# Kernel optimization log

Hardware: AMD Instinct MI355X
Metric: run time of the kernel (lower is better)

The kernel has to match this reference:

```python
import jax, jax.numpy as jnp
from jax import lax
import numpy as np

# dims
V, D, T = 30000, 300, 24          # vocab, glove dim, seq len
H = 256                            # tweet_out_size == z_dim
NT, NU = 6000, 4000                # tweet nodes, user nodes
N = NT + NU
F, Z = 512, 256                    # user_feat_size, z_dim
E = 80000
B = 2000                           # batch_size (source tweets)
H1, H2, HEADS = 64, 100, 8
NEG = 0.2                          # GATConv default negative_slope


def setup_inputs() -> dict:
    k = jax.random.split(jax.random.key(0), 32)
    r = lambda i, shape, s=0.05: (s * jax.random.normal(k[i], shape)).astype(jnp.float32)
    return {
        "user_text": jax.random.randint(k[0], (B, T), 0, V),
        "user_feats": jax.random.normal(k[1], (NU, F), jnp.float32),
        "graph_node_features": jax.random.randint(k[2], (NT, T), 0, V),
        "graph_edge_index": jax.random.randint(k[3], (2, E), 0, N),
        "tweet_emb": r(4, (V, D), 0.1),
        "w_ih0": r(5, (3 * H, D)), "w_hh0": r(6, (3 * H, H)),
        "b_ih0": r(7, (3 * H,)), "b_hh0": r(8, (3 * H,)),
        "w_ih1": r(9, (3 * H, H)), "w_hh1": r(10, (3 * H, H)),
        "b_ih1": r(11, (3 * H,)), "b_hh1": r(12, (3 * H,)),
        "h0": r(13, (2, NT, H), 1.0),
        "w_mu": r(14, (Z, F)), "b_mu": r(15, (Z,)),
        "w_lv": r(16, (Z, F)), "b_lv": r(17, (Z,)),
        "w_dec": r(18, (F, Z)), "b_dec": r(19, (F,)),
        "vae_eps": r(20, (NU, Z), 1.0),
        "w1": r(21, (H, HEADS * H1)), "a_src1": r(22, (HEADS, H1)),
        "a_dst1": r(23, (HEADS, H1)), "b1": r(24, (HEADS * H1,)),
        "w2": r(25, (HEADS * H1, H2)), "a_src2": r(26, (1, H2)),
        "a_dst2": r(27, (1, H2)), "b2": r(28, (H2,)),
    }


def _gru_layer(x_seq, h0, w_ih, w_hh, b_ih, b_hh):
    # x_seq: [T, B, in]; torch nn.GRU gate math
    def step(h, x):
        gi = x @ w_ih.T + b_ih
        gh = h @ w_hh.T + b_hh
        i_r, i_z, i_n = jnp.split(gi, 3, axis=-1)
        h_r, h_z, h_n = jnp.split(gh, 3, axis=-1)
        r = jax.nn.sigmoid(i_r + h_r)
        z = jax.nn.sigmoid(i_z + h_z)
        n = jnp.tanh(i_n + r * h_n)
        hn = (1.0 - z) * n + z * h
        return hn, hn
    h_last, out = lax.scan(step, h0, x_seq)
    return out, h_last


def _gat(x, src, dst, w, a_src, a_dst, bias, heads, out_ch, concat):
    # PyG GATConv (eval mode, self-loops already appended)
    n = x.shape[0]
    xp = (x @ w).reshape(n, heads, out_ch)          # [N, H, C]
    as_n = (xp * a_src).sum(-1)                     # [N, H]
    ad_n = (xp * a_dst).sum(-1)
    e = jax.nn.leaky_relu(as_n[src] + ad_n[dst], NEG)          # [E, H]
    emax = jax.ops.segment_max(e, dst, num_segments=n)         # edge-softmax over dst
    ee = jnp.exp(e - emax[dst])
    denom = jax.ops.segment_sum(ee, dst, num_segments=n)
    alpha = ee / denom[dst]
    out = jax.ops.segment_sum(xp[src] * alpha[:, :, None], dst, num_segments=n)
    out = out.reshape(n, heads * out_ch) if concat else out.mean(axis=1)
    return out + bias


def reference(user_text, user_feats, graph_node_features, graph_edge_index,
              tweet_emb, w_ih0, w_hh0, b_ih0, b_hh0, w_ih1, w_hh1, b_ih1, b_hh1,
              h0, w_mu, b_mu, w_lv, b_lv, w_dec, b_dec, vae_eps,
              w1, a_src1, a_dst1, b1, w2, a_src2, a_dst2, b2):
    # --- VAE user embedding ---
    mu = user_feats @ w_mu.T + b_mu
    logvar = user_feats @ w_lv.T + b_lv
    z = mu + jnp.exp(0.5 * logvar) * vae_eps        # reparameterized latent
    rec = z @ w_dec.T + b_dec
    kl_loss = (-0.5 * (1.0 + logvar - mu**2 - jnp.exp(logvar)).sum(-1)).mean()
    rec_loss = ((rec - user_feats) ** 2).mean()
    # --- tweet encoder: embedding lookup + 2-layer GRU ---
    xe = tweet_emb[graph_node_features].transpose(1, 0, 2)     # [T, NT, D]
    out0, _ = _gru_layer(xe, h0[0], w_ih0, w_hh0, b_ih0, b_hh0)
    _, hn = _gru_layer(out0, h0[1], w_ih1, w_hh1, b_ih1, b_hh1)  # [NT, H]
    # --- assemble node features: source tweets, users, other tweets ---
    x_in = jnp.concatenate([hn[:B], z, hn[B:]], axis=0)        # [N, H]
    loops = jnp.arange(x_in.shape[0])
    src = jnp.concatenate([graph_edge_index[0], loops])
    dst = jnp.concatenate([graph_edge_index[1], loops])
    x1 = _gat(x_in, src, dst, w1, a_src1, a_dst1, b1, HEADS, H1, True)
    x2 = _gat(x1, src, dst, w2, a_src2, a_dst2, b2, 1, H2, False)
    return x2, kl_loss, rec_loss
```

## Files before the change

### kernel.cpp

```cpp
#include <hip/hip_runtime.h>

#define V_ 30000
#define D_ 300
#define DP_ 320
#define T_ 24
#define H_ 256
#define NT_ 6000
#define NU_ 4000
#define N_ 10000
#define F_ 512
#define Z_ 256
#define E_ 80000
#define B_ 2000
#define H1_ 64
#define H2_ 100
#define HEADS_ 8
#define E2_ (E_ + N_)

typedef __bf16 bf16_t;
typedef bf16_t bf16x8 __attribute__((ext_vector_type(8)));
typedef float  f32x4  __attribute__((ext_vector_type(4)));

__device__ __forceinline__ void gll16(const bf16_t* g, bf16_t* l)
{
    __builtin_amdgcn_global_load_lds(
        (const __attribute__((address_space(1))) void*)g,
        (__attribute__((address_space(3))) void*)l, 16, 0, 0);
}

struct GCfg {
    const bf16_t* A; const bf16_t* B; const float* bias;
    float* Cf; bf16_t* Cb; int M, N, K, ldc;
    const int* gtok; int t0;
};

template<bool OUTBF>
__global__ __launch_bounds__(256) void mfma_gemm(GCfg g0, GCfg g1)
{
    const GCfg g = blockIdx.z ? g1 : g0;
    __shared__ __align__(16) bf16_t SMEM[16384];
    const int tid  = (int)threadIdx.x;
    const int wave = tid >> 6, lane = tid & 63;
    const int quad = lane >> 4, l16 = lane & 15;
    const int mq = (wave & 1) * 64, nq = (wave >> 1) * 64;

    int bx = (int)blockIdx.x, by = (int)blockIdx.y;
    {
        int gx = (int)gridDim.x, total = gx * (int)gridDim.y;
        if ((total & 7) == 0) {
            int L = by * gx + bx;
            int F = (L & 7) * (total >> 3) + (L >> 3);
            bx = F % gx;
            by = F / gx;
        }
    }
    const int mbase = by * 128, nbase = bx * 128;
    const int M = g.M, N = g.N, K = g.K, ldc = g.ldc;

    const bf16_t* agp[2];
    const bf16_t* bgp[2];
#pragma unroll
    for (int j = 0; j < 2; j++) {
        int i = wave * 128 + j * 64 + lane;
        int c = i >> 7, row = i & 127;
        int r = mbase + row; if (r >= M) r = M - 1;
        int src = g.gtok ? g.gtok[(r % NT_) * T_ + g.t0 + (r / NT_)] : r;
        agp[j] = g.A + (size_t)src * K + c * 8;
        int rb = nbase + row; if (rb >= N) rb = N - 1;
        bgp[j] = g.B + (size_t)rb * K + c * 8;
    }

    f32x4 acc[4][4];
#pragma unroll
    for (int mi = 0; mi < 4; mi++)
#pragma unroll
        for (int ni = 0; ni < 4; ni++) acc[mi][ni] = (f32x4){0.f, 0.f, 0.f, 0.f};

    auto stage = [&](int b, int k0) {
        bf16_t* ab = SMEM + b * 4096 + wave * 1024;
        bf16_t* bb = SMEM + 8192 + b * 4096 + wave * 1024;
        gll16(agp[0] + k0, ab);
        gll16(agp[1] + k0, ab + 512);
        gll16(bgp[0] + k0, bb);
        gll16(bgp[1] + k0, bb + 512);
    };

    const int niter = K >> 5;
    stage(0, 0);
    for (int ks = 0; ks < niter; ks++) {
        __syncthreads();
        if (ks + 1 < niter) stage((ks + 1) & 1, (ks + 1) * 32);
        const bf16_t* Ab = SMEM + (ks & 1) * 4096;
        const bf16_t* Bb = SMEM + 8192 + (ks & 1) * 4096;
        bf16x8 afr[4], bfr[4];
#pragma unroll
        for (int mi = 0; mi < 4; mi++)
            afr[mi] = *(const bf16x8*)(Ab + (size_t)(quad * 128 + mq + mi * 16 + l16) * 8);
#pragma unroll
        for (int ni = 0; ni < 4; ni++)
            bfr[ni] = *(const bf16x8*)(Bb + (size_t)(quad * 128 + nq + ni * 16 + l16) * 8);
#pragma unroll
        for (int mi = 0; mi < 4; mi++)
#pragma unroll
            for (int ni = 0; ni < 4; ni++)
                acc[mi][ni] = __builtin_amdgcn_mfma_f32_16x16x32_bf16(
                    afr[mi], bfr[ni], acc[mi][ni], 0, 0, 0);
    }

    if (OUTBF) {
        __syncthreads();
#pragma unroll
        for (int ni = 0; ni < 4; ni++) {
            int colc = nq + ni * 16 + l16;
            float bv = g.bias ? g.bias[nbase + colc] : 0.f;
            int cc = colc >> 3, off = colc & 7;
#pragma unroll
            for (int mi = 0; mi < 4; mi++)
#pragma unroll
                for (int r = 0; r < 4; r++) {
                    int row = mq + mi * 16 + quad * 4 + r;
                    int sw = (row ^ (row >> 3)) & 7;
                    SMEM[row * 128 + ((cc ^ sw) << 3) + off] =
                        (bf16_t)(acc[mi][ni][r] + bv);
                }
        }
        __syncthreads();
        {
            int row = tid >> 1, seg = tid & 1;
            int sw = (row ^ (row >> 3)) & 7;
            int growr = mbase + row;
            if (growr < M) {
#pragma unroll
                for (int q = 0; q < 8; q++) {
                    int cc = seg * 8 + q;
                    bf16x8 v = *(const bf16x8*)(SMEM + row * 128 + ((cc ^ sw) << 3));
                    *(bf16x8*)(g.Cb + (size_t)growr * ldc + nbase + cc * 8) = v;
                }
            }
        }
    } else {
#pragma unroll
        for (int ni = 0; ni < 4; ni++) {
            int col = nbase + nq + ni * 16 + l16;
            if (col >= N) continue;
            float bv = g.bias ? g.bias[col] : 0.f;
#pragma unroll
            for (int mi = 0; mi < 4; mi++)
#pragma unroll
                for (int r = 0; r < 4; r++) {
                    int row = mbase + mq + mi * 16 + quad * 4 + r;
                    if (row >= M) continue;
                    g.Cf[(size_t)row * ldc + col] = acc[mi][ni][r] + bv;
                }
        }
    }
}

struct MegaLay {
    const bf16_t* temb;
    const int*    gnf;
    const bf16_t* wih0;
    const bf16_t* whh0;
    const bf16_t* wih1;
    const bf16_t* whh1;
    const float *bih0, *bhh0, *bih1, *bhh1;
    const bf16_t* h0in;
    const bf16_t* h1in;
    bf16_t*       h1out;
};

__device__ __forceinline__ float rcp_(float x)
{
    float r;
    asm("v_rcp_f32 %0, %1" : "=v"(r) : "v"(x));
    return r;
}
__device__ __forceinline__ float sigm_(float x)
{
    return rcp_(1.f + __expf(-x));
}
__device__ __forceinline__ float tanh_(float x)
{
    x = fminf(fmaxf(x, -15.f), 15.f);
    float t = __expf(2.f * x);
    return 1.f - 2.f * rcp_(t + 1.f);
}

#define HSW(Hb, row, byte) ((char*)(Hb) + ((((row) * 512) + (byte)) ^ (((row) & 7) << 4)))

__global__ __launch_bounds__(512, 1) void gru_mega(MegaLay L)
{
    __shared__ __align__(16) bf16_t H0L[8192];
    __shared__ __align__(16) bf16_t H1L[8192];
    __shared__ __align__(16) bf16_t XE[20480];
    __shared__ int TOK[768];
    const int tid  = (int)threadIdx.x;
    const int wv   = tid >> 6, lane = tid & 63;
    const int quad = lane >> 4, l16 = lane & 15;
    const int row0 = (int)blockIdx.x * 32;

    for (int i = tid; i < 768; i += 512) {
        int gi = row0 * T_ + i; if (gi >= NT_ * T_) gi = NT_ * T_ - 1;
        TOK[i] = L.gnf[gi];
    }
#pragma unroll
    for (int i = 0; i < 2; i++) {
        int idx  = i * 512 + tid;
        int rowl = idx >> 5, seg = idx & 31;
        int grow = row0 + rowl; if (grow >= NT_) grow = NT_ - 1;
        *(bf16x8*)HSW(H0L, rowl, seg * 16) =
            *(const bf16x8*)(L.h0in + (size_t)grow * H_ + seg * 8);
        *(bf16x8*)HSW(H1L, rowl, seg * 16) =
            *(const bf16x8*)(L.h1in + (size_t)grow * H_ + seg * 8);
    }

    float brz0[2][2], bni0[2], bnh0[2], brz1[2][2], bni1[2], bnh1[2];
#pragma unroll
    for (int jj = 0; jj < 2; jj++) {
        int col = wv * 32 + jj * 16 + l16;
        brz0[0][jj] = L.bih0[col] + L.bhh0[col];
        brz0[1][jj] = L.bih0[256 + col] + L.bhh0[256 + col];
        bni0[jj]    = L.bih0[512 + col];
        bnh0[jj]    = L.bhh0[512 + col];
        brz1[0][jj] = L.bih1[col] + L.bhh1[col];
        brz1[1][jj] = L.bih1[256 + col] + L.bhh1[256 + col];
        bni1[jj]    = L.bih1[512 + col];
        bnh1[jj]    = L.bhh1[512 + col];
    }

    auto gather = [&](int t) {
        bf16_t* xb = XE + (t & 1) * 10240;
#pragma unroll
        for (int k = 0; k < 3; k++) {
            int i = wv + k * 8;
            if (i < 20) {
                int flat = i * 64 + lane;
                int row  = flat / 40;
                int s    = flat - row * 40;
                int c4   = s ^ (row & 7);
                int tok  = TOK[row * T_ + t];
                gll16(L.temb + (size_t)tok * DP_ + c4 * 8, xb + i * 512 + lane * 8);
            }
        }
    };

    auto run_gemm = [&](auto&& loadA, const bf16_t* W, int nks,
                        f32x4 (&arz)[2][2][2], f32x4 (&an)[2][2]) {
        bf16x8 bA[3][2], bB[3][2];
        auto loadB = [&](bf16x8 (&b)[3][2], int ks) {
#pragma unroll
            for (int g = 0; g < 3; g++)
#pragma unroll
                for (int jj = 0; jj < 2; jj++)
                    b[g][jj] = *(const bf16x8*)(W +
                        (((size_t)(g * 16 + wv * 2 + jj) * nks + ks) << 9) + lane * 8);
        };
        auto mstep = [&](bf16x8 (&b)[3][2], int ks) {
            bf16x8 afr[2];
            loadA(afr, ks);
#pragma unroll
            for (int m = 0; m < 2; m++)
#pragma unroll
                for (int jj = 0; jj < 2; jj++) {
                    arz[m][0][jj] = __builtin_amdgcn_mfma_f32_16x16x32_bf16(
                        afr[m], b[0][jj], arz[m][0][jj], 0, 0, 0);
                    arz[m][1][jj] = __builtin_amdgcn_mfma_f32_16x16x32_bf16(
                        afr[m], b[1][jj], arz[m][1][jj], 0, 0, 0);
                    an[m][jj] = __builtin_amdgcn_mfma_f32_16x16x32_bf16(
                        afr[m], b[2][jj], an[m][jj], 0, 0, 0);
                }
        };
        loadB(bA, 0);
#pragma unroll 1
        for (int kp = 0; kp < nks; kp += 2) {
            loadB(bB, kp + 1);
            mstep(bA, kp);
            if (kp + 2 < nks) loadB(bA, kp + 2);
            mstep(bB, kp + 1);
        }
    };

    __syncthreads();
    gather(0);

    for (int t = 0; t < T_; t++) {
        __syncthreads();
        if (t + 1 < T_) gather(t + 1);

        f32x4 arz[2][2][2], an_i[2][2], an_h[2][2];
#pragma unroll
        for (int m = 0; m < 2; m++)
#pragma unroll
            for (int jj = 0; jj < 2; jj++) {
                arz[m][0][jj] = (f32x4){0.f, 0.f, 0.f, 0.f};
                arz[m][1][jj] = (f32x4){0.f, 0.f, 0.f, 0.f};
                an_i[m][jj]   = (f32x4){0.f, 0.f, 0.f, 0.f};
                an_h[m][jj]   = (f32x4){0.f, 0.f, 0.f, 0.f};
            }

        {
            const bf16_t* xb = XE + (t & 1) * 10240;
            run_gemm([&](bf16x8* afr, int ks) {
#pragma unroll
                for (int m = 0; m < 2; m++) {
                    int row = m * 16 + l16;
                    afr[m] = *(const bf16x8*)(xb + row * DP_ +
                               (((ks * 4 + quad) ^ (row & 7)) << 3));
                }
            }, L.wih0, 10, arz, an_i);
            run_gemm([&](bf16x8* afr, int ks) {
#pragma unroll
                for (int m = 0; m < 2; m++)
                    afr[m] = *(const bf16x8*)HSW(H0L, m * 16 + l16,
                                                 ks * 64 + quad * 16);
            }, L.whh0, 8, arz, an_h);
        }
        __syncthreads();

#pragma unroll
        for (int m = 0; m < 2; m++)
#pragma unroll
            for (int jj = 0; jj < 2; jj++) {
                int col = wv * 32 + jj * 16 + l16;
#pragma unroll
                for (int r = 0; r < 4; r++) {
                    int rowl = m * 16 + quad * 4 + r;
                    float hold = (float)*(const bf16_t*)HSW(H0L, rowl, col * 2);
                    float rg = sigm_(arz[m][0][jj][r] + brz0[0][jj]);
                    float zg = sigm_(arz[m][1][jj][r] + brz0[1][jj]);
                    float ng = tanh_(an_i[m][jj][r] + bni0[jj] +
                                     rg * (an_h[m][jj][r] + bnh0[jj]));
                    *(bf16_t*)HSW(H0L, rowl, col * 2) =
                        (bf16_t)((1.f - zg) * ng + zg * hold);
                }
            }
        __syncthreads();

#pragma unroll
        for (int m = 0; m < 2; m++)
#pragma unroll
            for (int jj = 0; jj < 2; jj++) {
                arz[m][0][jj] = (f32x4){0.f, 0.f, 0.f, 0.f};
                arz[m][1][jj] = (f32x4){0.f, 0.f, 0.f, 0.f};
                an_i[m][jj]   = (f32x4){0.f, 0.f, 0.f, 0.f};
                an_h[m][jj]   = (f32x4){0.f, 0.f, 0.f, 0.f};
            }
        run_gemm([&](bf16x8* afr, int ks) {
#pragma unroll
            for (int m = 0; m < 2; m++)
                afr[m] = *(const bf16x8*)HSW(H0L, m * 16 + l16,
                                             ks * 64 + quad * 16);
        }, L.wih1, 8, arz, an_i);
        run_gemm([&](bf16x8* afr, int ks) {
#pragma unroll
            for (int m = 0; m < 2; m++)
                afr[m] = *(const bf16x8*)HSW(H1L, m * 16 + l16,
                                             ks * 64 + quad * 16);
        }, L.whh1, 8, arz, an_h);
        __syncthreads();

#pragma unroll
        for (int m = 0; m < 2; m++)
#pragma unroll
            for (int jj = 0; jj < 2; jj++) {
                int col = wv * 32 + jj * 16 + l16;
#pragma unroll
                for (int r = 0; r < 4; r++) {
                    int rowl = m * 16 + quad * 4 + r;
                    float hold = (float)*(const bf16_t*)HSW(H1L, rowl, col * 2);
                    float rg = sigm_(arz[m][0][jj][r] + brz1[0][jj]);
                    float zg = sigm_(arz[m][1][jj][r] + brz1[1][jj]);
                    float ng = tanh_(an_i[m][jj][r] + bni1[jj] +
                                     rg * (an_h[m][jj][r] + bnh1[jj]));
                    *(bf16_t*)HSW(H1L, rowl, col * 2) =
                        (bf16_t)((1.f - zg) * ng + zg * hold);
                }
            }
    }

    __syncthreads();
#pragma unroll
    for (int i = 0; i < 2; i++) {
        int idx  = i * 512 + tid;
        int rowl = idx >> 5, seg = idx & 31;
        int grow = row0 + rowl;
        if (grow < NT_) {
            bf16x8 v = *(const bf16x8*)HSW(H1L, rowl, seg * 16);
            *(bf16x8*)(L.h1out + (size_t)grow * H_ + seg * 8) = v;
        }
    }
}

struct SegD { const float* src; bf16_t* dst; int rows, cin, cout, transp; };
struct PrepArgs { SegD seg[11]; long long base[12]; int nseg; long long total; };

__global__ void prep_kern(PrepArgs pa)
{
    long long stride = (long long)gridDim.x * blockDim.x;
    for (long long i = (long long)blockIdx.x * blockDim.x + threadIdx.x;
         i < pa.total; i += stride) {
        int k = 0;
        while (k + 1 < pa.nseg && i >= pa.base[k + 1]) k++;
        long long local = i - pa.base[k];
        SegD sg = pa.seg[k];
        float v;
        if (sg.transp == 2) {
            int nks  = sg.cout >> 5;
            int o    = (int)local;
            int e    = o & 7;
            int lane = (o >> 3) & 63;
            int rest = o >> 9;
            int ks   = rest % nks;
            int gcb  = rest / nks;
            int r    = (gcb >> 4) * 256 + (gcb & 15) * 16 + (lane & 15);
            int kk   = ks * 32 + (lane >> 4) * 8 + e;
            v = (kk < sg.cin) ? sg.src[(size_t)r * sg.cin + kk] : 0.f;
        } else {
            int r = (int)(local / sg.cout);
            int c = (int)(local - (long long)r * sg.cout);
            if (sg.transp) v = sg.src[(size_t)c * sg.rows + r];
            else           v = (c < sg.cin) ? sg.src[(size_t)r * sg.cin + c] : 0.f;
        }
        sg.dst[local] = (bf16_t)v;
    }
}

__global__ void init_all(const float* __restrict__ h0in, bf16_t* __restrict__ h0b,
                         bf16_t* __restrict__ h1b,
                         int* __restrict__ deg, int* __restrict__ dcnt,
                         float* __restrict__ loss2, float* __restrict__ b_ml,
                         const float* __restrict__ b_mu, const float* __restrict__ b_lv)
{
    int i = blockIdx.x * blockDim.x + threadIdx.x;
    if (i < NT_ * H_) {
        h0b[i] = (bf16_t)h0in[i];
        h1b[i] = (bf16_t)h0in[NT_ * H_ + i];
    }
    if (i < N_) { deg[i] = 0; dcnt[i] = 0; }
    if (i < 2 * Z_) b_ml[i] = (i < Z_) ? b_mu[i] : b_lv[i - Z_];
    if (i < 2) loss2[i] = 0.f;
}

__device__ __forceinline__ void edge_sd(const int* __restrict__ ei, int e, int& s, int& d)
{
    if (e < E_) { s = ei[e]; d = ei[E_ + e]; }
    else        { s = d = e - E_; }
}

__global__ void csr_hist(const int* __restrict__ ei, int* __restrict__ deg)
{
    int e = blockIdx.x * blockDim.x + threadIdx.x;
    if (e >= E2_) return;
    int s, d; edge_sd(ei, e, s, d);
    atomicAdd(deg + d, 1);
}

__global__ void csr_scan(const int* __restrict__ deg, int* __restrict__ rowptr)
{
    __shared__ int buf[256];
    __shared__ int carry;
    int tid = (int)threadIdx.x;
    if (tid == 0) { carry = 0; rowptr[0] = 0; }
    __syncthreads();
    for (int c0 = 0; c0 < N_; c0 += 256) {
        int i = c0 + tid;
        buf[tid] = (i < N_) ? deg[i] : 0;
        __syncthreads();
        for (int off = 1; off < 256; off <<= 1) {
            int t = (tid >= off) ? buf[tid - off] : 0;
            __syncthreads();
            buf[tid] += t;
            __syncthreads();
        }
        if (i < N_) rowptr[i + 1] = carry + buf[tid];
        __syncthreads();
        if (tid == 255) carry += buf[255];
        __syncthreads();
    }
}

__global__ void csr_scatter(const int* __restrict__ ei, const int* __restrict__ rowptr,
                            int* __restrict__ dcnt, int* __restrict__ csrc)
{
    int e = blockIdx.x * blockDim.x + threadIdx.x;
    if (e >= E2_) return;
    int s, d; edge_sd(ei, e, s, d);
    int pos = rowptr[d] + atomicAdd(dcnt + d, 1);
    csrc[pos] = s;
}

__global__ __launch_bounds__(256) void vae_z_kl(
    const float* __restrict__ ml, const float* __restrict__ eps,
    bf16_t* __restrict__ z_out, float* __restrict__ kl_out)
{
    float t = 0.f;
    int stride = (int)gridDim.x * 256;
    for (int idx = blockIdx.x * 256 + threadIdx.x; idx < NU_ * Z_; idx += stride) {
        int row = idx >> 8, c = idx & 255;
        float m = ml[(size_t)row * 512 + c];
        float l = ml[(size_t)row * 512 + 256 + c];
        float el = expf(l);
        z_out[idx] = (bf16_t)(m + expf(0.5f * l) * eps[idx]);
        t += -0.5f * (1.f + l - m * m - el);
    }
    __shared__ float red[256];
    red[threadIdx.x] = t;
    __syncthreads();
    for (int s = 128; s > 0; s >>= 1) {
        if ((int)threadIdx.x < s) red[threadIdx.x] += red[threadIdx.x + s];
        __syncthreads();
    }
    if (threadIdx.x == 0) atomicAdd(kl_out, red[0] * (1.f / NU_));
}

__global__ __launch_bounds__(256) void rec_loss_kern(
    const float* __restrict__ rec, const float* __restrict__ uf,
    float* __restrict__ loss_out)
{
    float t = 0.f;
    int stride = (int)gridDim.x * 256;
    for (int idx = blockIdx.x * 256 + threadIdx.x; idx < NU_ * F_; idx += stride) {
        float d = rec[idx] - uf[idx];
        t += d * d;
    }
    __shared__ float red[256];
    red[threadIdx.x] = t;
    __syncthreads();
    for (int s = 128; s > 0; s >>= 1) {
        if ((int)threadIdx.x < s) red[threadIdx.x] += red[threadIdx.x + s];
        __syncthreads();
    }
    if (threadIdx.x == 0) atomicAdd(loss_out, red[0] * (1.f / (NU_ * F_)));
}

__global__ void assemble_xin(const bf16_t* __restrict__ h1, bf16_t* __restrict__ x_in)
{
    int idx = blockIdx.x * blockDim.x + threadIdx.x;
    if (idx >= NT_ * H_) return;
    int row = idx >> 8, col = idx & 255;
    int dst = (row < B_) ? row : (row + NU_);
    x_in[(size_t)dst * H_ + col] = h1[idx];
}

__global__ void gat_attn_coef_bf(const bf16_t* __restrict__ xp,
                                 const float* __restrict__ a_src,
                                 const float* __restrict__ a_dst,
                                 float* __restrict__ asn, float* __restrict__ adn,
                                 int heads, int C)
{
    int i = blockIdx.x * blockDim.x + threadIdx.x;
    if (i >= N_ * heads) return;
    int node = i / heads, h = i - node * heads;
    const bf16_t* x = xp + (size_t)(node * heads + h) * C;
    float s = 0.f, d = 0.f;
    for (int c8 = 0; c8 < C; c8 += 8) {
        bf16x8 v = *(const bf16x8*)(x + c8);
#pragma unroll
        for (int j = 0; j < 8; j++) {
            float vv = (float)v[j];
            s += vv * a_src[h * C + c8 + j];
            d += vv * a_dst[h * C + c8 + j];
        }
    }
    asn[i] = s;
    adn[i] = d;
}

__global__ void gat_attn_coef(const float* __restrict__ xp, const float* __restrict__ a_src,
                              const float* __restrict__ a_dst, float* __restrict__ asn,
                              float* __restrict__ adn, int heads, int C)
{
    int i = blockIdx.x * blockDim.x + threadIdx.x;
    if (i >= N_ * heads) return;
    int node = i / heads, h = i - node * heads;
    const float* x = xp + (size_t)(node * heads + h) * C;
    float s = 0.f, d = 0.f;
    for (int c = 0; c < C; c++) {
        float v = x[c];
        s += v * a_src[h * C + c];
        d += v * a_dst[h * C + c];
    }
    asn[i] = s;
    adn[i] = d;
}

__global__ __launch_bounds__(256) void gat_agg1(
    const int* __restrict__ rowptr, const int* __restrict__ csrc,
    const float* __restrict__ asn, const float* __restrict__ adn,
    const bf16_t* __restrict__ xp, const float* __restrict__ bias,
    bf16_t* __restrict__ x1out)
{
    int d = blockIdx.x;
    int tid = (int)threadIdx.x;
    int beg = rowptr[d], end = rowptr[d + 1];
    int h0 = tid >> 6, h1 = h0 + 4;
    float ad0 = adn[d * 8 + h0], ad1 = adn[d * 8 + h1];
    float mx0 = -1e30f, mx1 = -1e30f;
    for (int e = beg; e < end; e++) {
        int s = csrc[e];
        float l0 = asn[s * 8 + h0] + ad0; l0 = (l0 > 0.f) ? l0 : 0.2f * l0;
        float l1 = asn[s * 8 + h1] + ad1; l1 = (l1 > 0.f) ? l1 : 0.2f * l1;
        mx0 = fmaxf(mx0, l0); mx1 = fmaxf(mx1, l1);
    }
    float den0 = 0.f, den1 = 0.f, acc0 = 0.f, acc1 = 0.f;
    for (int e = beg; e < end; e++) {
        int s = csrc[e];
        float l0 = asn[s * 8 + h0] + ad0; l0 = (l0 > 0.f) ? l0 : 0.2f * l0;
        float l1 = asn[s * 8 + h1] + ad1; l1 = (l1 > 0.f) ? l1 : 0.2f * l1;
        float p0 = expf(l0 - mx0), p1 = expf(l1 - mx1);
        den0 += p0; den1 += p1;
        acc0 += p0 * (float)xp[(size_t)s * 512 + tid];
        acc1 += p1 * (float)xp[(size_t)s * 512 + 256 + tid];
    }
    x1out[(size_t)d * 512 + tid]       = (bf16_t)(bias[tid] + acc0 / den0);
    x1out[(size_t)d * 512 + 256 + tid] = (bf16_t)(bias[256 + tid] + acc1 / den1);
}

__global__ __launch_bounds__(256) void gat_agg2(
    const int* __restrict__ rowptr, const int* __restrict__ csrc,
    const float* __restrict__ asn, const float* __restrict__ adn,
    const float* __restrict__ xp, const float* __restrict__ bias,
    float* __restrict__ outp)
{
    int d = blockIdx.x * 4 + ((int)threadIdx.x >> 6);
    if (d >= N_) return;
    int lane = (int)threadIdx.x & 63;
    int beg = rowptr[d], end = rowptr[d + 1];
    float adnd = adn[d];
    float mx = -1e30f;
    for (int e = beg; e < end; e++) {
        float l = asn[csrc[e]] + adnd;
        l = (l > 0.f) ? l : 0.2f * l;
        mx = fmaxf(mx, l);
    }
    float den = 0.f, acc0 = 0.f, acc1 = 0.f;
    for (int e = beg; e < end; e++) {
        int s = csrc[e];
        float l = asn[s] + adnd;
        l = (l > 0.f) ? l : 0.2f * l;
        float p = expf(l - mx);
        den += p;
        acc0 += p * xp[(size_t)s * H2_ + lane];
        if (lane < H2_ - 64) acc1 += p * xp[(size_t)s * H2_ + 64 + lane];
    }
    outp[(size_t)d * H2_ + lane] = bias[lane] + acc0 / den;
    if (lane < H2_ - 64)
        outp[(size_t)d * H2_ + 64 + lane] = bias[64 + lane] + acc1 / den;
}

extern "C" void kernel_launch(void* const* d_in, const int* in_sizes, int n_in,
                              void* d_out, int out_size, void* d_ws, size_t ws_size,
                              hipStream_t stream)
{
    const float* user_feats = (const float*)d_in[1];
    const int*   gnf        = (const int*)d_in[2];
    const int*   ei         = (const int*)d_in[3];
    const float* temb       = (const float*)d_in[4];
    const float* w_ih0      = (const float*)d_in[5];
    const float* w_hh0      = (const float*)d_in[6];
    const float* b_ih0      = (const float*)d_in[7];
    const float* b_hh0      = (const float*)d_in[8];
    const float* w_ih1      = (const float*)d_in[9];
    const float* w_hh1      = (const float*)d_in[10];
    const float* b_ih1      = (const float*)d_in[11];
    const float* b_hh1      = (const float*)d_in[12];
    const float* h0in       = (const float*)d_in[13];
    const float* w_mu       = (const float*)d_in[14];
    const float* b_mu       = (const float*)d_in[15];
    const float* w_lv       = (const float*)d_in[16];
    const float* b_lv       = (const float*)d_in[17];
    const float* w_dec      = (const float*)d_in[18];
    const float* b_dec      = (const float*)d_in[19];
    const float* veps       = (const float*)d_in[20];
    const float* w1         = (const float*)d_in[21];
    const float* a_src1     = (const float*)d_in[22];
    const float* a_dst1     = (const float*)d_in[23];
    const float* b1         = (const float*)d_in[24];
    const float* w2         = (const float*)d_in[25];
    const float* a_src2     = (const float*)d_in[26];
    const float* a_dst2     = (const float*)d_in[27];
    const float* b2         = (const float*)d_in[28];
    float* out = (float*)d_out;

    char* wsb = (char*)d_ws;
    bf16_t* temb_bf = (bf16_t*)(wsb + 0);
    float*  mlbuf   = (float*)(wsb + 56064000);
    float*  recb    = (float*)(wsb + 64256000);
    bf16_t* xp1b    = (bf16_t*)(wsb + 0);
    bf16_t* x1b     = (bf16_t*)(wsb + 20480000);
    float*  xp2     = (float*)(wsb + 30720000);
    bf16_t* wih0_bf = (bf16_t*)(wsb + 92928000);
    bf16_t* whh0_bf = (bf16_t*)(wsb + 93419520);
    bf16_t* wih1_bf = (bf16_t*)(wsb + 93812736);
    bf16_t* whh1_bf = (bf16_t*)(wsb + 94205952);
    bf16_t* wml_bf  = (bf16_t*)(wsb + 94599168);
    bf16_t* wdec_bf = (bf16_t*)(wsb + 95123456);
    bf16_t* w1t_bf  = (bf16_t*)(wsb + 95385600);
    bf16_t* w2t_bf  = (bf16_t*)(wsb + 95648000);
    float*  b_ml    = (float*)(wsb + 95750400);
    bf16_t* ufeats_bf = (bf16_t*)(wsb + 95752448);
    bf16_t* h0b_init = (bf16_t*)(wsb + 124424448);
    bf16_t* h1init  = (bf16_t*)(wsb + 127496448);
    bf16_t* h1sA    = (bf16_t*)(wsb + 130568448);
    bf16_t* xin_bf  = (bf16_t*)(wsb + 136712448);
    int*    deg     = (int*)(wsb + 141832448);
    int*    dcnt    = (int*)(wsb + 141872448);
    int*    rowptr  = (int*)(wsb + 141912448);
    int*    csrc    = (int*)(wsb + 141952512);
    float*  asn1    = (float*)(wsb + 142312512);
    float*  adn1    = (float*)(wsb + 142632512);
    float*  asn2    = (float*)(wsb + 142952512);
    float*  adn2    = (float*)(wsb + 142992512);

    const int TB = 256;
    auto blocks = [](int n) { return (n + 255) / 256; };

    auto mkcfg = [](const bf16_t* A, const bf16_t* B, const float* bias,
                    float* Cf, bf16_t* Cb, int M, int N, int K, int ldc,
                    const int* gtok, int t0) {
        GCfg g; g.A = A; g.B = B; g.bias = bias; g.Cf = Cf; g.Cb = Cb;
        g.M = M; g.N = N; g.K = K; g.ldc = ldc; g.gtok = gtok; g.t0 = t0;
        return g;
    };
    auto launch_bf = [&](GCfg g0) {
        dim3 grid((g0.N + 127) / 128, (g0.M + 127) / 128, 1);
        hipLaunchKernelGGL((mfma_gemm<true>), grid, dim3(TB), 0, stream, g0, g0);
    };
    auto launch_f32 = [&](GCfg g0) {
        dim3 grid((g0.N + 127) / 128, (g0.M + 127) / 128, 1);
        hipLaunchKernelGGL((mfma_gemm<false>), grid, dim3(TB), 0, stream, g0, g0);
    };

    PrepArgs pa;
    auto seg = [&](int k, const float* s, bf16_t* dst, int rows, int cin, int cout, int tr) {
        pa.seg[k] = SegD{s, dst, rows, cin, cout, tr};
    };
    seg(0, temb, temb_bf, V_, D_, DP_, 0);
    seg(1, w_ih0, wih0_bf, 3 * H_, D_, DP_, 2);
    seg(2, w_hh0, whh0_bf, 3 * H_, H_, H_, 2);
    seg(3, w_ih1, wih1_bf, 3 * H_, H_, H_, 2);
    seg(4, w_hh1, whh1_bf, 3 * H_, H_, H_, 2);
    seg(5, w_mu, wml_bf, Z_, F_, F_, 0);
    seg(6, w_lv, wml_bf + (size_t)Z_ * F_, Z_, F_, F_, 0);
    seg(7, w_dec, wdec_bf, F_, Z_, Z_, 0);
    seg(8, user_feats, ufeats_bf, NU_, F_, F_, 0);
    seg(9, w1, w1t_bf, HEADS_ * H1_, 0, H_, 1);
    seg(10, w2, w2t_bf, H2_, 0, HEADS_ * H1_, 1);
    pa.nseg = 11;
    long long acc = 0;
    for (int k = 0; k < 11; k++) {
        pa.base[k] = acc;
        acc += (long long)pa.seg[k].rows * pa.seg[k].cout;
    }
    pa.base[11] = acc;
    pa.total = acc;
    hipLaunchKernelGGL(prep_kern, dim3(6144), dim3(TB), 0, stream, pa);

    hipLaunchKernelGGL(init_all, dim3(blocks(NT_ * H_)), dim3(TB), 0, stream,
                       h0in, h0b_init, h1init,
                       deg, dcnt, out + N_ * H2_, b_ml, b_mu, b_lv);

    hipLaunchKernelGGL(csr_hist, dim3(blocks(E2_)), dim3(TB), 0, stream, ei, deg);
    hipLaunchKernelGGL(csr_scan, dim3(1), dim3(TB), 0, stream, deg, rowptr);
    hipLaunchKernelGGL(csr_scatter, dim3(blocks(E2_)), dim3(TB), 0, stream,
                       ei, rowptr, dcnt, csrc);

    launch_f32(mkcfg(ufeats_bf, wml_bf, b_ml, mlbuf, nullptr,
                     NU_, 2 * Z_, F_, 2 * Z_, nullptr, 0));
    bf16_t* z_bf = xin_bf + (size_t)B_ * H_;
    hipLaunchKernelGGL(vae_z_kl, dim3(256), dim3(TB), 0, stream,
                       mlbuf, veps, z_bf, out + N_ * H2_);
    launch_f32(mkcfg(z_bf, wdec_bf, b_dec, recb, nullptr,
                     NU_, F_, Z_, F_, nullptr, 0));
    hipLaunchKernelGGL(rec_loss_kern, dim3(256), dim3(TB), 0, stream,
                       recb, user_feats, out + N_ * H2_ + 1);

    {
        MegaLay ML;
        ML.temb = temb_bf; ML.gnf = gnf;
        ML.wih0 = wih0_bf; ML.whh0 = whh0_bf;
        ML.wih1 = wih1_bf; ML.whh1 = whh1_bf;
        ML.bih0 = b_ih0; ML.bhh0 = b_hh0; ML.bih1 = b_ih1; ML.bhh1 = b_hh1;
        ML.h0in = h0b_init; ML.h1in = h1init; ML.h1out = h1sA;
        hipLaunchKernelGGL(gru_mega, dim3((NT_ + 31) / 32), dim3(512), 0, stream, ML);
    }

    hipLaunchKernelGGL(assemble_xin, dim3(blocks(NT_ * H_)), dim3(TB), 0, stream,
                       h1sA, xin_bf);

    launch_bf(mkcfg(xin_bf, w1t_bf, nullptr, nullptr, xp1b,
                    N_, HEADS_ * H1_, H_, HEADS_ * H1_, nullptr, 0));
    hipLaunchKernelGGL(gat_attn_coef_bf, dim3(blocks(N_ * HEADS_)), dim3(TB), 0, stream,
                       xp1b, a_src1, a_dst1, asn1, adn1, HEADS_, H1_);
    hipLaunchKernelGGL(gat_agg1, dim3(N_), dim3(TB), 0, stream,
                       rowptr, csrc, asn1, adn1, xp1b, b1, x1b);

    launch_f32(mkcfg(x1b, w2t_bf, nullptr, xp2, nullptr,
                     N_, H2_, HEADS_ * H1_, H2_, nullptr, 0));
    hipLaunchKernelGGL(gat_attn_coef, dim3(blocks(N_)), dim3(TB), 0, stream,
                       xp2, a_src2, a_dst2, asn2, adn2, 1, H2_);
    hipLaunchKernelGGL(gat_agg2, dim3((N_ + 3) / 4), dim3(TB), 0, stream,
                       rowptr, csrc, asn2, adn2, xp2, b2, out);

    (void)in_sizes; (void)n_in; (void)out_size; (void)ws_size;
}
```

Before: 840.8 us.

## Split GRU megakernel work across 16 waves per block instead of 8

The fused GRU kernel now runs 1024 threads per block, and each of the 16 waves owns a single 16-column slice instead of two. Per-wave accumulators, weight fragments and gate epilogues shrink by half. The aim is to put more waves in flight to hide the latency of the serial per-step GEMMs and gate math. In exchange, the A fragments are reloaded from LDS twice as often, and barriers now synchronise more waves.

```diff
diff --git a/kernel.cpp b/kernel.cpp
--- a/kernel.cpp
+++ b/kernel.cpp
@@ -188,7 +188,7 @@
 
 #define HSW(Hb, row, byte) ((char*)(Hb) + ((((row) * 512) + (byte)) ^ (((row) & 7) << 4)))
 
-__global__ __launch_bounds__(512, 1) void gru_mega(MegaLay L)
+__global__ __launch_bounds__(1024, 4) void gru_mega(MegaLay L)
 {
     __shared__ __align__(16) bf16_t H0L[8192];
     __shared__ __align__(16) bf16_t H1L[8192];
@@ -199,14 +199,12 @@
     const int quad = lane >> 4, l16 = lane & 15;
     const int row0 = (int)blockIdx.x * 32;
 
-    for (int i = tid; i < 768; i += 512) {
-        int gi = row0 * T_ + i; if (gi >= NT_ * T_) gi = NT_ * T_ - 1;
-        TOK[i] = L.gnf[gi];
-    }
-#pragma unroll
-    for (int i = 0; i < 2; i++) {
-        int idx  = i * 512 + tid;
-        int rowl = idx >> 5, seg = idx & 31;
+    if (tid < 768) {
+        int gi = row0 * T_ + tid; if (gi >= NT_ * T_) gi = NT_ * T_ - 1;
+        TOK[tid] = L.gnf[gi];
+    }
+    {
+        int rowl = tid >> 5, seg = tid & 31;
         int grow = row0 + rowl; if (grow >= NT_) grow = NT_ - 1;
         *(bf16x8*)HSW(H0L, rowl, seg * 16) =
             *(const bf16x8*)(L.h0in + (size_t)grow * H_ + seg * 8);
@@ -214,25 +212,24 @@
             *(const bf16x8*)(L.h1in + (size_t)grow * H_ + seg * 8);
     }
 
-    float brz0[2][2], bni0[2], bnh0[2], brz1[2][2], bni1[2], bnh1[2];
-#pragma unroll
-    for (int jj = 0; jj < 2; jj++) {
-        int col = wv * 32 + jj * 16 + l16;
-        brz0[0][jj] = L.bih0[col] + L.bhh0[col];
-        brz0[1][jj] = L.bih0[256 + col] + L.bhh0[256 + col];
-        bni0[jj]    = L.bih0[512 + col];
-        bnh0[jj]    = L.bhh0[512 + col];
-        brz1[0][jj] = L.bih1[col] + L.bhh1[col];
-        brz1[1][jj] = L.bih1[256 + col] + L.bhh1[256 + col];
-        bni1[jj]    = L.bih1[512 + col];
-        bnh1[jj]    = L.bhh1[512 + col];
+    float brz0[2], bni0, bnh0, brz1[2], bni1, bnh1;
+    {
+        int col = wv * 16 + l16;
+        brz0[0] = L.bih0[col] + L.bhh0[col];
+        brz0[1] = L.bih0[256 + col] + L.bhh0[256 + col];
+        bni0    = L.bih0[512 + col];
+        bnh0    = L.bhh0[512 + col];
+        brz1[0] = L.bih1[col] + L.bhh1[col];
+        brz1[1] = L.bih1[256 + col] + L.bhh1[256 + col];
+        bni1    = L.bih1[512 + col];
+        bnh1    = L.bhh1[512 + col];
     }
 
     auto gather = [&](int t) {
         bf16_t* xb = XE + (t & 1) * 10240;
 #pragma unroll
-        for (int k = 0; k < 3; k++) {
-            int i = wv + k * 8;
+        for (int k = 0; k < 2; k++) {
+            int i = wv + k * 16;
             if (i < 20) {
                 int flat = i * 64 + lane;
                 int row  = flat / 40;
@@ -245,30 +242,26 @@
     };
 
     auto run_gemm = [&](auto&& loadA, const bf16_t* W, int nks,
-                        f32x4 (&arz)[2][2][2], f32x4 (&an)[2][2]) {
-        bf16x8 bA[3][2], bB[3][2];
-        auto loadB = [&](bf16x8 (&b)[3][2], int ks) {
+                        f32x4 (&arz)[2][2], f32x4 (&an)[2]) {
+        bf16x8 bA[3], bB[3];
+        auto loadB = [&](bf16x8 (&b)[3], int ks) {
 #pragma unroll
             for (int g = 0; g < 3; g++)
-#pragma unroll
-                for (int jj = 0; jj < 2; jj++)
-                    b[g][jj] = *(const bf16x8*)(W +
-                        (((size_t)(g * 16 + wv * 2 + jj) * nks + ks) << 9) + lane * 8);
+                b[g] = *(const bf16x8*)(W +
+                    (((size_t)(g * 16 + wv) * nks + ks) << 9) + lane * 8);
         };
-        auto mstep = [&](bf16x8 (&b)[3][2], int ks) {
+        auto mstep = [&](bf16x8 (&b)[3], int ks) {
             bf16x8 afr[2];
             loadA(afr, ks);
 #pragma unroll
-            for (int m = 0; m < 2; m++)
-#pragma unroll
-                for (int jj = 0; jj < 2; jj++) {
-                    arz[m][0][jj] = __builtin_amdgcn_mfma_f32_16x16x32_bf16(
-                        afr[m], b[0][jj], arz[m][0][jj], 0, 0, 0);
-                    arz[m][1][jj] = __builtin_amdgcn_mfma_f32_16x16x32_bf16(
-                        afr[m], b[1][jj], arz[m][1][jj], 0, 0, 0);
-                    an[m][jj] = __builtin_amdgcn_mfma_f32_16x16x32_bf16(
-                        afr[m], b[2][jj], an[m][jj], 0, 0, 0);
-                }
+            for (int m = 0; m < 2; m++) {
+                arz[m][0] = __builtin_amdgcn_mfma_f32_16x16x32_bf16(
+                    afr[m], b[0], arz[m][0], 0, 0, 0);
+                arz[m][1] = __builtin_amdgcn_mfma_f32_16x16x32_bf16(
+                    afr[m], b[1], arz[m][1], 0, 0, 0);
+                an[m] = __builtin_amdgcn_mfma_f32_16x16x32_bf16(
+                    afr[m], b[2], an[m], 0, 0, 0);
+            }
         };
         loadB(bA, 0);
 #pragma unroll 1
@@ -287,16 +280,14 @@
         __syncthreads();
         if (t + 1 < T_) gather(t + 1);
 
-        f32x4 arz[2][2][2], an_i[2][2], an_h[2][2];
-#pragma unroll
-        for (int m = 0; m < 2; m++)
-#pragma unroll
-            for (int jj = 0; jj < 2; jj++) {
-                arz[m][0][jj] = (f32x4){0.f, 0.f, 0.f, 0.f};
-                arz[m][1][jj] = (f32x4){0.f, 0.f, 0.f, 0.f};
-                an_i[m][jj]   = (f32x4){0.f, 0.f, 0.f, 0.f};
-                an_h[m][jj]   = (f32x4){0.f, 0.f, 0.f, 0.f};
-            }
+        f32x4 arz[2][2], an_i[2], an_h[2];
+#pragma unroll
+        for (int m = 0; m < 2; m++) {
+            arz[m][0] = (f32x4){0.f, 0.f, 0.f, 0.f};
+            arz[m][1] = (f32x4){0.f, 0.f, 0.f, 0.f};
+            an_i[m]   = (f32x4){0.f, 0.f, 0.f, 0.f};
+            an_h[m]   = (f32x4){0.f, 0.f, 0.f, 0.f};
+        }
 
         {
             const bf16_t* xb = XE + (t & 1) * 10240;
@@ -318,33 +309,28 @@
         __syncthreads();
 
 #pragma unroll
-        for (int m = 0; m < 2; m++)
-#pragma unroll
-            for (int jj = 0; jj < 2; jj++) {
-                int col = wv * 32 + jj * 16 + l16;
-#pragma unroll
-                for (int r = 0; r < 4; r++) {
-                    int rowl = m * 16 + quad * 4 + r;
-                    float hold = (float)*(const bf16_t*)HSW(H0L, rowl, col * 2);
-                    float rg = sigm_(arz[m][0][jj][r] + brz0[0][jj]);
-                    float zg = sigm_(arz[m][1][jj][r] + brz0[1][jj]);
-                    float ng = tanh_(an_i[m][jj][r] + bni0[jj] +
-                                     rg * (an_h[m][jj][r] + bnh0[jj]));
-                    *(bf16_t*)HSW(H0L, rowl, col * 2) =
-                        (bf16_t)((1.f - zg) * ng + zg * hold);
-                }
+        for (int m = 0; m < 2; m++) {
+            int col = wv * 16 + l16;
+#pragma unroll
+            for (int r = 0; r < 4; r++) {
+                int rowl = m * 16 + quad * 4 + r;
+                float hold = (float)*(const bf16_t*)HSW(H0L, rowl, col * 2);
+                float rg = sigm_(arz[m][0][r] + brz0[0]);
+                float zg = sigm_(arz[m][1][r] + brz0[1]);
+                float ng = tanh_(an_i[m][r] + bni0 + rg * (an_h[m][r] + bnh0));
+                *(bf16_t*)HSW(H0L, rowl, col * 2) =
+                    (bf16_t)((1.f - zg) * ng + zg * hold);
             }
-        __syncthreads();
-
-#pragma unroll
-        for (int m = 0; m < 2; m++)
-#pragma unroll
-            for (int jj = 0; jj < 2; jj++) {
-                arz[m][0][jj] = (f32x4){0.f, 0.f, 0.f, 0.f};
-                arz[m][1][jj] = (f32x4){0.f, 0.f, 0.f, 0.f};
-                an_i[m][jj]   = (f32x4){0.f, 0.f, 0.f, 0.f};
-                an_h[m][jj]   = (f32x4){0.f, 0.f, 0.f, 0.f};
-            }
+        }
+        __syncthreads();
+
+#pragma unroll
+        for (int m = 0; m < 2; m++) {
+            arz[m][0] = (f32x4){0.f, 0.f, 0.f, 0.f};
+            arz[m][1] = (f32x4){0.f, 0.f, 0.f, 0.f};
+            an_i[m]   = (f32x4){0.f, 0.f, 0.f, 0.f};
+            an_h[m]   = (f32x4){0.f, 0.f, 0.f, 0.f};
+        }
         run_gemm([&](bf16x8* afr, int ks) {
 #pragma unroll
             for (int m = 0; m < 2; m++)
@@ -360,29 +346,24 @@
         __syncthreads();
 
 #pragma unroll
-        for (int m = 0; m < 2; m++)
-#pragma unroll
-            for (int jj = 0; jj < 2; jj++) {
-                int col = wv * 32 + jj * 16 + l16;
-#pragma unroll
-                for (int r = 0; r < 4; r++) {
-                    int rowl = m * 16 + quad * 4 + r;
-                    float hold = (float)*(const bf16_t*)HSW(H1L, rowl, col * 2);
-                    float rg = sigm_(arz[m][0][jj][r] + brz1[0][jj]);
-                    float zg = sigm_(arz[m][1][jj][r] + brz1[1][jj]);
-                    float ng = tanh_(an_i[m][jj][r] + bni1[jj] +
-                                     rg * (an_h[m][jj][r] + bnh1[jj]));
-                    *(bf16_t*)HSW(H1L, rowl, col * 2) =
-                        (bf16_t)((1.f - zg) * ng + zg * hold);
-                }
+        for (int m = 0; m < 2; m++) {
+            int col = wv * 16 + l16;
+#pragma unroll
+            for (int r = 0; r < 4; r++) {
+                int rowl = m * 16 + quad * 4 + r;
+                float hold = (float)*(const bf16_t*)HSW(H1L, rowl, col * 2);
+                float rg = sigm_(arz[m][0][r] + brz1[0]);
+                float zg = sigm_(arz[m][1][r] + brz1[1]);
+                float ng = tanh_(an_i[m][r] + bni1 + rg * (an_h[m][r] + bnh1));
+                *(bf16_t*)HSW(H1L, rowl, col * 2) =
+                    (bf16_t)((1.f - zg) * ng + zg * hold);
             }
+        }
     }
 
     __syncthreads();
-#pragma unroll
-    for (int i = 0; i < 2; i++) {
-        int idx  = i * 512 + tid;
-        int rowl = idx >> 5, seg = idx & 31;
+    {
+        int rowl = tid >> 5, seg = tid & 31;
         int grow = row0 + rowl;
         if (grow < NT_) {
             bf16x8 v = *(const bf16x8*)HSW(H1L, rowl, seg * 16);
@@ -782,7 +763,7 @@
         ML.wih1 = wih1_bf; ML.whh1 = whh1_bf;
         ML.bih0 = b_ih0; ML.bhh0 = b_hh0; ML.bih1 = b_ih1; ML.bhh1 = b_hh1;
         ML.h0in = h0b_init; ML.h1in = h1init; ML.h1out = h1sA;
-        hipLaunchKernelGGL(gru_mega, dim3((NT_ + 31) / 32), dim3(512), 0, stream, ML);
+        hipLaunchKernelGGL(gru_mega, dim3((NT_ + 31) / 32), dim3(1024), 0, stream, ML);
     }
 
     hipLaunchKernelGGL(assemble_xin, dim3(blocks(NT_ * H_)), dim3(TB), 0, stream,
```

Result: slower. 859.2 us (+2.2%).
